# Optimization experiments

Hardware: AMD Instinct MI355X
Metric: run time of the kernel (lower is better)

## Reference

```python
import jax, jax.numpy as jnp
import numpy as np

N_NODES = 50000
N_EDGES = 800000
IN_DIM = 2
EDGE_DIM = 2
HIDDEN = 64
N_LAYERS = 3
MAX_LEAKS = 3


def setup_inputs() -> dict:
    key = jax.random.key(0)
    ks = iter(jax.random.split(key, 32))
    s = 0.05
    inp = {
        "x": jax.random.normal(next(ks), (N_NODES, IN_DIM), dtype=jnp.float32),
        "edge_index": jax.random.randint(next(ks), (2, N_EDGES), 0, N_NODES, dtype=jnp.int32),
        "edge_attr": jax.random.normal(next(ks), (N_EDGES, EDGE_DIM), dtype=jnp.float32),
        # input projection
        "W_in": jax.random.normal(next(ks), (IN_DIM, HIDDEN), dtype=jnp.float32) * s,
        "b_in": jnp.zeros((HIDDEN,), jnp.float32),
        # message-passing layers (stacked over L)
        "W_msg": jax.random.normal(next(ks), (N_LAYERS, HIDDEN + EDGE_DIM, HIDDEN), dtype=jnp.float32) * s,
        "b_msg": jnp.zeros((N_LAYERS, HIDDEN), jnp.float32),
        "W_upd": jax.random.normal(next(ks), (N_LAYERS, 2 * HIDDEN, HIDDEN), dtype=jnp.float32) * s,
        "b_upd": jnp.zeros((N_LAYERS, HIDDEN), jnp.float32),
        # per-node leak-logit head
        "W_node": jax.random.normal(next(ks), (HIDDEN, 1), dtype=jnp.float32) * s,
        "b_node": jnp.zeros((1,), jnp.float32),
        # global no-leak head
        "W_pool": jax.random.normal(next(ks), (HIDDEN, 1), dtype=jnp.float32) * s,
        "b_pool": jnp.zeros((1,), jnp.float32),
        # num_leaks head: Linear(H, H//2) -> ReLU -> Linear(H//2, max_leaks+1)
        "W_h1": jax.random.normal(next(ks), (HIDDEN, HIDDEN // 2), dtype=jnp.float32) * s,
        "b_h1": jnp.zeros((HIDDEN // 2,), jnp.float32),
        "W_h2": jax.random.normal(next(ks), (HIDDEN // 2, MAX_LEAKS + 1), dtype=jnp.float32) * s,
        "b_h2": jnp.zeros((MAX_LEAKS + 1,), jnp.float32),
    }
    return inp


def _run_gnn(x, src, dst, edge_attr, W_in, b_in, W_msg, b_msg, W_upd, b_upd):
    """input_proj + num_layers of message passing; returns node embeddings h [N, H]."""
    n_nodes = x.shape[0]
    h = x @ W_in + b_in  # [N, H]
    # in-degree for mean aggregation (clamped to avoid div-by-zero)
    deg = jax.ops.segment_sum(jnp.ones((src.shape[0],), h.dtype), dst, num_segments=n_nodes)
    deg = jnp.maximum(deg, 1.0)[:, None]  # [N, 1]
    for l in range(N_LAYERS):
        # message: MLP over [h_src || edge_attr], gathered along edges
        m = jax.nn.relu(jnp.concatenate([h[src], edge_attr], axis=-1) @ W_msg[l] + b_msg[l])  # [E, H]
        agg = jax.ops.segment_sum(m, dst, num_segments=n_nodes) / deg  # [N, H]
        # update: MLP over [h || agg]
        h = jax.nn.relu(jnp.concatenate([h, agg], axis=-1) @ W_upd[l] + b_upd[l])  # [N, H]
    return h


def reference(x, edge_index, edge_attr, W_in, b_in, W_msg, b_msg, W_upd, b_upd,
              W_node, b_node, W_pool, b_pool, W_h1, b_h1, W_h2, b_h2):
    src, dst = edge_index[0], edge_index[1]
    # base GNN forward (dropout is identity at inference)
    h = _run_gnn(x, src, dst, edge_attr, W_in, b_in, W_msg, b_msg, W_upd, b_upd)  # [N, H]
    node_logits = (h @ W_node + b_node)[:, 0]          # [N]
    node_probs = jax.nn.sigmoid(node_logits)           # [N]
    # the multi-leak forward re-runs input_proj + mp_layers; identical math -> reuse h
    h_global = jnp.mean(h, axis=0, keepdims=True)      # [1, H]
    num_leaks_logits = jax.nn.relu(h_global @ W_h1 + b_h1) @ W_h2 + b_h2  # [1, max_leaks+1]
    return node_probs, num_leaks_logits, h
```

## Files before the change

kernel.cpp:

```cpp
#include <hip/hip_runtime.h>
#include <math.h>

constexpr int H = 64;

typedef __attribute__((ext_vector_type(8))) short bf16x8;
typedef __attribute__((ext_vector_type(4))) float f32x4;
typedef unsigned long long u64;

__device__ inline unsigned short f2bf(float f) {
  union { float f; unsigned int u; } c; c.f = f;
  unsigned int u = c.u;
  return (unsigned short)((u + 0x7FFF + ((u >> 16) & 1)) >> 16);
}
__device__ inline float bf2f(unsigned int s) {
  union { unsigned int u; float f; } c; c.u = s << 16;
  return c.f;
}
__device__ inline unsigned char f2fp8(float f) {
  return (unsigned char)(__builtin_amdgcn_cvt_pk_fp8_f32(f, f, 0, false) & 0xFF);
}

__global__ void k_prep(int* __restrict__ hist, float* __restrict__ hsumP,
                       const float* __restrict__ Wmsg, const float* __restrict__ Wupd,
                       unsigned short* __restrict__ WmT, unsigned short* __restrict__ WuT,
                       int n) {
  int t = blockIdx.x * blockDim.x + threadIdx.x;
  if (t < n) hist[t] = 0;
  if (t < 512) hsumP[t] = 0.f;
  int u = t - n;
  if (u >= 0 && u < 3 * 12288) {
    int l = u / 12288, rem = u % 12288;
    if (rem < 4096) {
      int j = rem >> 6, k = rem & 63;
      WmT[l * 4096 + rem] = f2bf(Wmsg[(size_t)l * 66 * 64 + k * 64 + j]);
    } else {
      int r2 = rem - 4096;
      int j = r2 >> 7, k = r2 & 127;
      WuT[l * 8192 + r2] = f2bf(Wupd[(size_t)l * 128 * 64 + k * 64 + j]);
    }
  }
}

__global__ void k_hist(const int* __restrict__ dst, int* __restrict__ hist, int E) {
  int e = blockIdx.x * blockDim.x + threadIdx.x;
  if (e < E) atomicAdd(&hist[dst[e]], 1);
}

__global__ void k_scan1(const int* __restrict__ hist, int* __restrict__ bsum, int n) {
  __shared__ int sred[256];
  int tid = threadIdx.x;
  int base = blockIdx.x * 1024 + tid * 4;
  int s = 0;
#pragma unroll
  for (int k = 0; k < 4; ++k) { int i = base + k; if (i < n) s += hist[i]; }
  sred[tid] = s;
  __syncthreads();
  for (int d = 128; d > 0; d >>= 1) {
    if (tid < d) sred[tid] += sred[tid + d];
    __syncthreads();
  }
  if (tid == 0) bsum[blockIdx.x] = sred[0];
}

__global__ void k_scan2(int* __restrict__ bsum, int* __restrict__ bcur, int nb) {
  __shared__ int sd[1024];
  int tid = threadIdx.x;
  int v = (tid < nb) ? bsum[tid] : 0;
  sd[tid] = v;
  __syncthreads();
  for (int d = 1; d < 1024; d <<= 1) {
    int t = (tid >= d) ? sd[tid - d] : 0;
    __syncthreads();
    sd[tid] += t;
    __syncthreads();
  }
  if (tid < nb) {
    int ex = sd[tid] - v;
    bsum[tid] = ex;
    bcur[tid] = ex;
  }
}

__global__ void k_scan3(const int* __restrict__ hist, const int* __restrict__ bsum,
                        int* __restrict__ row_ptr, int* __restrict__ pos, int n) {
  __shared__ int sth[256];
  int tid = threadIdx.x;
  int base = blockIdx.x * 1024 + tid * 4;
  int v[4]; int s = 0;
#pragma unroll
  for (int k = 0; k < 4; ++k) { int i = base + k; v[k] = (i < n) ? hist[i] : 0; s += v[k]; }
  sth[tid] = s;
  __syncthreads();
  for (int d = 1; d < 256; d <<= 1) {
    int t = (tid >= d) ? sth[tid - d] : 0;
    __syncthreads();
    sth[tid] += t;
    __syncthreads();
  }
  int run = bsum[blockIdx.x] + sth[tid] - s;
  if (blockIdx.x == 0 && tid == 0) row_ptr[0] = 0;
#pragma unroll
  for (int k = 0; k < 4; ++k) {
    int i = base + k;
    if (i < n) {
      pos[i] = run;
      run += v[k];
      row_ptr[i + 1] = run;
    }
  }
}

__global__ void k_part(const int* __restrict__ src, const int* __restrict__ dst,
                       const float2* __restrict__ ea2, int* __restrict__ bcur,
                       u64* __restrict__ staged, int E, int B) {
  __shared__ u64 srt[2048];
  __shared__ int cnt[64], offs[64], gbase[64];
  int tid = threadIdx.x;
  int base = blockIdx.x * 2048;
  if (tid < 64) cnt[tid] = 0;
  __syncthreads();
  u64 rec_[8]; int bk_[8], rk_[8];
#pragma unroll
  for (int k = 0; k < 8; ++k) {
    int e = base + k * 256 + tid;
    if (e < E) {
      int d = dst[e];
      int bk = d >> 10;
      float2 eav = ea2[e];
      unsigned int eap = (unsigned int)f2bf(eav.x) | ((unsigned int)f2bf(eav.y) << 16);
      rec_[k] = (u64)(unsigned int)(src[e] & 0xFFFF)
              | ((u64)(unsigned int)(d & 1023) << 16)
              | ((u64)(unsigned int)bk << 26)
              | ((u64)eap << 32);
      bk_[k] = bk;
      rk_[k] = atomicAdd(&cnt[bk], 1);
    } else bk_[k] = -1;
  }
  __syncthreads();
  if (tid == 0) {
    int run = 0;
    for (int b = 0; b < B; ++b) { offs[b] = run; run += cnt[b]; }
  }
  __syncthreads();
#pragma unroll
  for (int k = 0; k < 8; ++k)
    if (bk_[k] >= 0) srt[offs[bk_[k]] + rk_[k]] = rec_[k];
  __syncthreads();
  if (tid < B && cnt[tid] > 0) gbase[tid] = atomicAdd(&bcur[tid], cnt[tid]);
  __syncthreads();
  int total = (base + 2048 <= E) ? 2048 : (E > base ? E - base : 0);
  for (int i = tid; i < total; i += 256) {
    u64 r = srt[i];
    int bk = (int)((r >> 26) & 63u);
    staged[gbase[bk] + (i - offs[bk])] = r;
  }
}

__global__ void k_place(const u64* __restrict__ staged, const int* __restrict__ rptr,
                        u64* __restrict__ erec, int N_) {
  __shared__ int cnt2[1024];
  __shared__ int rptrL[1025];
  int b = blockIdx.x;
  int nd0 = b << 10;
  int nn = min(nd0 + 1024, N_) - nd0;
  int tid = threadIdx.x;
  if (tid < nn) { cnt2[tid] = 0; rptrL[tid] = rptr[nd0 + tid]; }
  if (tid == 0) rptrL[nn] = rptr[nd0 + nn];
  __syncthreads();
  int beg = rptrL[0], end = rptrL[nn];
  for (int i = beg + tid; i < end; i += 1024) {
    u64 r = staged[i];
    int dl = (int)((r >> 16) & 1023u);
    int p = rptrL[dl] + atomicAdd(&cnt2[dl], 1);
    erec[p] = (r & 0xFFFFull) | ((r >> 32) << 32);
  }
}

__global__ void k_scatter(const int* __restrict__ src, const int* __restrict__ dst,
                          const float* __restrict__ ea, int* __restrict__ pos,
                          u64* __restrict__ erec, int E) {
  int e = blockIdx.x * blockDim.x + threadIdx.x;
  if (e < E) {
    int d = dst[e];
    int p = atomicAdd(&pos[d], 1);
    u64 lo = f2bf(ea[2 * e]);
    u64 hi = f2bf(ea[2 * e + 1]);
    erec[p] = (u64)(unsigned int)src[e] | ((lo | (hi << 16)) << 32);
  }
}

__global__ void k_inproj_gemm(const float* __restrict__ x, const float* __restrict__ Win,
                              const float* __restrict__ bin,
                              const unsigned short* __restrict__ wmt,
                              unsigned short* __restrict__ hb,
                              unsigned char* __restrict__ g, int n) {
  int lane = threadIdx.x & 63;
  int wv = blockIdx.x * (blockDim.x >> 6) + (threadIdx.x >> 6);
  int v0 = wv * 16;
  if (v0 >= n) return;
  int r16 = lane & 15, hi = lane >> 4;
  int row = v0 + r16;
  float x0 = 0.f, x1 = 0.f;
  if (row < n) { x0 = x[2 * row]; x1 = x[2 * row + 1]; }
  union { bf16x8 v; unsigned short u[8]; } af[2];
#pragma unroll
  for (int s = 0; s < 2; ++s)
#pragma unroll
    for (int t = 0; t < 8; ++t) {
      int j = s * 32 + hi * 8 + t;
      af[s].u[t] = f2bf(fmaf(x0, Win[j], fmaf(x1, Win[64 + j], bin[j])));
    }
  if (row < n) {
    *(bf16x8*)(hb + (size_t)row * H + hi * 8)      = af[0].v;
    *(bf16x8*)(hb + (size_t)row * H + 32 + hi * 8) = af[1].v;
  }
  bf16x8 bfr[2][4];
#pragma unroll
  for (int ks = 0; ks < 2; ++ks)
#pragma unroll
    for (int jt = 0; jt < 4; ++jt)
      bfr[ks][jt] = *(const bf16x8*)(wmt + (jt * 16 + r16) * 64 + ks * 32 + hi * 8);
  f32x4 acc[4] = {};
#pragma unroll
  for (int ks = 0; ks < 2; ++ks)
#pragma unroll
    for (int jt = 0; jt < 4; ++jt)
      acc[jt] = __builtin_amdgcn_mfma_f32_16x16x32_bf16(af[ks].v, bfr[ks][jt], acc[jt], 0, 0, 0);
#pragma unroll
  for (int jt = 0; jt < 4; ++jt) {
    int col = jt * 16 + r16;
#pragma unroll
    for (int r = 0; r < 4; ++r) {
      int orow = v0 + hi * 4 + r;
      if (orow < n) g[(size_t)orow * H + col] = f2fp8(acc[jt][r]);
    }
  }
}

__device__ inline void acc8(float* a, uint2 gw, float e0, float e1,
                            const float4 waL, const float4 waH,
                            const float4 wbL, const float4 wbH,
                            const float4 bL, const float4 bH) {
  a[0] += fmaxf(fmaf(e0, waL.x, fmaf(e1, wbL.x, __builtin_amdgcn_cvt_f32_fp8(gw.x, 0) + bL.x)), 0.f);
  a[1] += fmaxf(fmaf(e0, waL.y, fmaf(e1, wbL.y, __builtin_amdgcn_cvt_f32_fp8(gw.x, 1) + bL.y)), 0.f);
  a[2] += fmaxf(fmaf(e0, waL.z, fmaf(e1, wbL.z, __builtin_amdgcn_cvt_f32_fp8(gw.x, 2) + bL.z)), 0.f);
  a[3] += fmaxf(fmaf(e0, waL.w, fmaf(e1, wbL.w, __builtin_amdgcn_cvt_f32_fp8(gw.x, 3) + bL.w)), 0.f);
  a[4] += fmaxf(fmaf(e0, waH.x, fmaf(e1, wbH.x, __builtin_amdgcn_cvt_f32_fp8(gw.y, 0) + bH.x)), 0.f);
  a[5] += fmaxf(fmaf(e0, waH.y, fmaf(e1, wbH.y, __builtin_amdgcn_cvt_f32_fp8(gw.y, 1) + bH.y)), 0.f);
  a[6] += fmaxf(fmaf(e0, waH.z, fmaf(e1, wbH.z, __builtin_amdgcn_cvt_f32_fp8(gw.y, 2) + bH.z)), 0.f);
  a[7] += fmaxf(fmaf(e0, waH.w, fmaf(e1, wbH.w, __builtin_amdgcn_cvt_f32_fp8(gw.y, 3) + bH.w)), 0.f);
}

__global__ void k_layer(const unsigned char* __restrict__ g_in,
                        const int* __restrict__ row_ptr, const u64* __restrict__ erec,
                        const float* __restrict__ Wm2, const float* __restrict__ bm,
                        unsigned short* __restrict__ hb,
                        const unsigned short* __restrict__ wut,
                        const float* __restrict__ bu,
                        const unsigned short* __restrict__ wmt_next,
                        unsigned char* __restrict__ g_out,
                        float* __restrict__ hout,
                        const float* __restrict__ Wn, const float* __restrict__ bn,
                        float* __restrict__ probs, float* __restrict__ hsumP,
                        int n) {
  __shared__ __align__(16) unsigned short aggL[64][72];
  __shared__ __align__(16) unsigned short hstage[4][16][72];
  __shared__ float shsum[64];
  int v0 = blockIdx.x * 64;

  {
    int gid = threadIdx.x >> 3, r = threadIdx.x & 7;
    int j0 = r * 8;
    float4 waL = *(const float4*)(Wm2 + j0);
    float4 waH = *(const float4*)(Wm2 + j0 + 4);
    float4 wbL = *(const float4*)(Wm2 + 64 + j0);
    float4 wbH = *(const float4*)(Wm2 + 64 + j0 + 4);
    float4 bL  = *(const float4*)(bm + j0);
    float4 bH  = *(const float4*)(bm + j0 + 4);
#pragma unroll
    for (int it = 0; it < 2; ++it) {
      int lv = it * 32 + gid;
      int v = v0 + lv;
      uint4 o = make_uint4(0, 0, 0, 0);
      if (v < n) {
        int beg = row_ptr[v], end = row_ptr[v + 1];
        float a[8] = {0.f, 0.f, 0.f, 0.f, 0.f, 0.f, 0.f, 0.f};
        int i = beg;
        for (; i + 3 < end; i += 4) {
          u64 rA = erec[i], rB = erec[i + 1], rC = erec[i + 2], rD = erec[i + 3];
          uint2 gwA = *(const uint2*)(g_in + (size_t)(unsigned int)rA * H + j0);
          uint2 gwB = *(const uint2*)(g_in + (size_t)(unsigned int)rB * H + j0);
          uint2 gwC = *(const uint2*)(g_in + (size_t)(unsigned int)rC * H + j0);
          uint2 gwD = *(const uint2*)(g_in + (size_t)(unsigned int)rD * H + j0);
          unsigned int eA = (unsigned int)(rA >> 32), eB = (unsigned int)(rB >> 32);
          unsigned int eC = (unsigned int)(rC >> 32), eD = (unsigned int)(rD >> 32);
          acc8(a, gwA, bf2f(eA & 0xffffu), bf2f(eA >> 16), waL, waH, wbL, wbH, bL, bH);
          acc8(a, gwB, bf2f(eB & 0xffffu), bf2f(eB >> 16), waL, waH, wbL, wbH, bL, bH);
          acc8(a, gwC, bf2f(eC & 0xffffu), bf2f(eC >> 16), waL, waH, wbL, wbH, bL, bH);
          acc8(a, gwD, bf2f(eD & 0xffffu), bf2f(eD >> 16), waL, waH, wbL, wbH, bL, bH);
        }
        for (; i < end; ++i) {
          u64 rA = erec[i];
          uint2 gwA = *(const uint2*)(g_in + (size_t)(unsigned int)rA * H + j0);
          unsigned int eA = (unsigned int)(rA >> 32);
          acc8(a, gwA, bf2f(eA & 0xffffu), bf2f(eA >> 16), waL, waH, wbL, wbH, bL, bH);
        }
        float inv = 1.f / fmaxf((float)(end - beg), 1.f);
        o.x = (unsigned int)f2bf(a[0] * inv) | ((unsigned int)f2bf(a[1] * inv) << 16);
        o.y = (unsigned int)f2bf(a[2] * inv) | ((unsigned int)f2bf(a[3] * inv) << 16);
        o.z = (unsigned int)f2bf(a[4] * inv) | ((unsigned int)f2bf(a[5] * inv) << 16);
        o.w = (unsigned int)f2bf(a[6] * inv) | ((unsigned int)f2bf(a[7] * inv) << 16);
      }
      *(uint4*)(&aggL[lv][j0]) = o;
    }
  }
  __syncthreads();

  int lane = threadIdx.x & 63;
  int w = threadIdx.x >> 6;
  int wv0 = v0 + w * 16;
  bool act = wv0 < n;
  int r16 = lane & 15, hi = lane >> 4;
  int lw = w * 16 + r16;
  if (hout && threadIdx.x < 64) shsum[threadIdx.x] = 0.f;
  bf16x8 bfr[4][4];
#pragma unroll
  for (int ks = 0; ks < 4; ++ks)
#pragma unroll
    for (int jt = 0; jt < 4; ++jt)
      bfr[ks][jt] = *(const bf16x8*)(wut + (jt * 16 + r16) * 128 + ks * 32 + hi * 8);
  f32x4 acc[4];
#pragma unroll
  for (int jt = 0; jt < 4; ++jt) {
    float b = bu[jt * 16 + r16];
    acc[jt] = (f32x4){b, b, b, b};
  }
  bf16x8 afr[4];
  int row = wv0 + r16;
  if (act && row < n) {
    const unsigned short* hrow = hb + (size_t)row * H + hi * 8;
    afr[0] = *(const bf16x8*)(hrow);
    afr[1] = *(const bf16x8*)(hrow + 32);
  } else {
    afr[0] = afr[1] = (bf16x8){0,0,0,0,0,0,0,0};
  }
  afr[2] = *(const bf16x8*)(&aggL[lw][hi * 8]);
  afr[3] = *(const bf16x8*)(&aggL[lw][32 + hi * 8]);
#pragma unroll
  for (int ks = 0; ks < 4; ++ks)
#pragma unroll
    for (int jt = 0; jt < 4; ++jt)
      acc[jt] = __builtin_amdgcn_mfma_f32_16x16x32_bf16(afr[ks], bfr[ks][jt], acc[jt], 0, 0, 0);
  float ov[4][4];
  unsigned short ob[4][4];
#pragma unroll
  for (int jt = 0; jt < 4; ++jt) {
    int col = jt * 16 + r16;
#pragma unroll
    for (int r = 0; r < 4; ++r) {
      int orow = wv0 + hi * 4 + r;
      bool ok = act && orow < n;
      float o = fmaxf(acc[jt][r], 0.f);
      ov[jt][r] = ok ? o : 0.f;
      ob[jt][r] = f2bf(ov[jt][r]);
      if (ok) {
        hb[(size_t)orow * H + col] = ob[jt][r];
        if (hout) hout[(size_t)orow * H + col] = o;
      }
    }
  }
  if (wmt_next) {
#pragma unroll
    for (int jt = 0; jt < 4; ++jt)
#pragma unroll
      for (int r = 0; r < 4; ++r)
        hstage[w][hi * 4 + r][jt * 16 + r16] = ob[jt][r];
    __syncthreads();
    bf16x8 af2[2];
    af2[0] = *(const bf16x8*)(&hstage[w][r16][hi * 8]);
    af2[1] = *(const bf16x8*)(&hstage[w][r16][32 + hi * 8]);
    bf16x8 bf2r[2][4];
#pragma unroll
    for (int ks = 0; ks < 2; ++ks)
#pragma unroll
      for (int jt = 0; jt < 4; ++jt)
        bf2r[ks][jt] = *(const bf16x8*)(wmt_next + (jt * 16 + r16) * 64 + ks * 32 + hi * 8);
    f32x4 acc2[4] = {};
#pragma unroll
    for (int ks = 0; ks < 2; ++ks)
#pragma unroll
      for (int jt = 0; jt < 4; ++jt)
        acc2[jt] = __builtin_amdgcn_mfma_f32_16x16x32_bf16(af2[ks], bf2r[ks][jt], acc2[jt], 0, 0, 0);
#pragma unroll
    for (int jt = 0; jt < 4; ++jt) {
      int col = jt * 16 + r16;
#pragma unroll
      for (int r = 0; r < 4; ++r) {
        int orow = wv0 + hi * 4 + r;
        if (act && orow < n) g_out[(size_t)orow * H + col] = f2fp8(acc2[jt][r]);
      }
    }
  } else {
    float bn0 = bn[0];
    float lg[4] = {0.f, 0.f, 0.f, 0.f};
#pragma unroll
    for (int jt = 0; jt < 4; ++jt) {
      float wn = Wn[jt * 16 + r16];
#pragma unroll
      for (int r = 0; r < 4; ++r) lg[r] = fmaf(ov[jt][r], wn, lg[r]);
    }
#pragma unroll
    for (int d = 1; d < 16; d <<= 1) {
#pragma unroll
      for (int r = 0; r < 4; ++r) lg[r] += __shfl_xor(lg[r], d);
    }
    if (r16 == 0) {
#pragma unroll
      for (int r = 0; r < 4; ++r) {
        int orow = wv0 + hi * 4 + r;
        if (act && orow < n) probs[orow] = 1.f / (1.f + expf(-(lg[r] + bn0)));
      }
    }
    __syncthreads();
#pragma unroll
    for (int jt = 0; jt < 4; ++jt) {
      float s = ov[jt][0] + ov[jt][1] + ov[jt][2] + ov[jt][3];
      s += __shfl_xor(s, 16); s += __shfl_xor(s, 32);
      if (hi == 0) atomicAdd(&shsum[jt * 16 + r16], s);
    }
    __syncthreads();
    if (threadIdx.x < 64)
      atomicAdd(&hsumP[((blockIdx.x & 7) << 6) + threadIdx.x], shsum[threadIdx.x]);
  }
}

__global__ void k_final(const float* __restrict__ hsumP,
                        const float* __restrict__ W1, const float* __restrict__ b1,
                        const float* __restrict__ W2, const float* __restrict__ b2,
                        float* __restrict__ out4, float n_nodes) {
  __shared__ float hmean[64];
  __shared__ float z1[32];
  int tid = threadIdx.x;
  if (tid < 64) {
    float s = 0.f;
#pragma unroll
    for (int b = 0; b < 8; ++b) s += hsumP[b * 64 + tid];
    hmean[tid] = s / n_nodes;
  }
  __syncthreads();
  if (tid < 32) {
    float a = b1[tid];
    for (int k = 0; k < 64; ++k) a = fmaf(hmean[k], W1[k * 32 + tid], a);
    z1[tid] = fmaxf(a, 0.f);
  }
  __syncthreads();
  if (tid < 4) {
    float a = b2[tid];
    for (int k = 0; k < 32; ++k) a = fmaf(z1[k], W2[k * 4 + tid], a);
    out4[tid] = a;
  }
}

extern "C" void kernel_launch(void* const* d_in, const int* in_sizes, int n_in,
                              void* d_out, int out_size, void* d_ws, size_t ws_size,
                              hipStream_t stream) {
  const float* x    = (const float*)d_in[0];
  const int*   ei   = (const int*)d_in[1];
  const float* ea   = (const float*)d_in[2];
  const float* Win  = (const float*)d_in[3];
  const float* bin  = (const float*)d_in[4];
  const float* Wmsg = (const float*)d_in[5];
  const float* bmsg = (const float*)d_in[6];
  const float* Wupd = (const float*)d_in[7];
  const float* bupd = (const float*)d_in[8];
  const float* Wn   = (const float*)d_in[9];
  const float* bn   = (const float*)d_in[10];
  const float* W1   = (const float*)d_in[13];
  const float* b1   = (const float*)d_in[14];
  const float* W2   = (const float*)d_in[15];
  const float* b2   = (const float*)d_in[16];

  const int N = in_sizes[0] / 2;
  const int E = in_sizes[1] / 2;
  const int* src = ei;
  const int* dst = ei + E;

  char* ws = (char*)d_ws;
  size_t off = 0;
  auto alloc = [&](size_t bytes) {
    void* p = ws + off;
    off = (off + bytes + 255) & ~(size_t)255;
    return p;
  };
  int*   hist = (int*)  alloc((size_t)N * 4);
  int*   rptr = (int*)  alloc((size_t)(N + 1) * 4);
  int*   pos  = (int*)  alloc((size_t)N * 4);
  int*   bsum = (int*)  alloc((size_t)1024 * 4);
  int*   bcur = (int*)  alloc((size_t)1024 * 4);
  u64*   staged = (u64*)alloc((size_t)E * 8);
  u64*   erec = (u64*)  alloc((size_t)E * 8);
  unsigned short* hb   = (unsigned short*)alloc((size_t)N * H * 2);
  unsigned char*  gA   = (unsigned char*) alloc((size_t)N * H);
  unsigned char*  gB   = (unsigned char*) alloc((size_t)N * H);
  unsigned short* WmT  = (unsigned short*)alloc((size_t)3 * 64 * 64 * 2);
  unsigned short* WuT  = (unsigned short*)alloc((size_t)3 * 64 * 128 * 2);
  float* hsumP = (float*)alloc(8 * 64 * 4);
  (void)ws_size;

  float* probs = (float*)d_out;
  float* out4  = probs + N;
  float* h     = out4 + 4;

  int eb = (E + 255) / 256;
  int sb = (N + 1023) / 1024;
  k_prep<<<(N + 3 * 12288 + 255) / 256, 256, 0, stream>>>(hist, hsumP, Wmsg, Wupd, WmT, WuT, N);
  k_hist<<<eb, 256, 0, stream>>>(dst, hist, E);
  k_scan1<<<sb, 256, 0, stream>>>(hist, bsum, N);
  k_scan2<<<1, 1024, 0, stream>>>(bsum, bcur, sb);
  k_scan3<<<sb, 256, 0, stream>>>(hist, bsum, rptr, pos, N);

  int B = (N + 1023) >> 10;
  if (B <= 64) {
    k_part<<<(E + 2047) / 2048, 256, 0, stream>>>(src, dst, (const float2*)ea,
                                                  bcur, staged, E, B);
    k_place<<<B, 1024, 0, stream>>>(staged, rptr, erec, N);
  } else {
    k_scatter<<<eb, 256, 0, stream>>>(src, dst, ea, pos, erec, E);
  }

  int tiles = (N + 15) / 16;
  int mb = (tiles + 3) / 4;
  k_inproj_gemm<<<mb, 256, 0, stream>>>(x, Win, bin, WmT, hb, gA, N);

  int lb = (N + 63) / 64;
  for (int l = 0; l < 3; ++l) {
    const unsigned char* gin = (l & 1) ? gB : gA;
    unsigned char* gout      = (l & 1) ? gA : gB;
    k_layer<<<lb, 256, 0, stream>>>(gin, rptr, erec,
                                    Wmsg + (size_t)l * 66 * 64 + 64 * 64,
                                    bmsg + (size_t)l * 64,
                                    hb, WuT + (size_t)l * 64 * 128,
                                    bupd + (size_t)l * 64,
                                    (l < 2) ? (WmT + (size_t)(l + 1) * 64 * 64) : nullptr,
                                    gout,
                                    (l == 2) ? h : nullptr,
                                    Wn, bn, probs, hsumP, N);
  }

  k_final<<<1, 64, 0, stream>>>(hsumP, W1, b1, W2, b2, out4, (float)N);
}
```

Before: 215.9 us.

## Fuse degree histogram into bucket partition and halve nodes per layer block

```diff
diff --git a/kernel.cpp b/kernel.cpp
--- a/kernel.cpp
+++ b/kernel.cpp
@@ -21,12 +21,14 @@
 }
 
 __global__ void k_prep(int* __restrict__ hist, float* __restrict__ hsumP,
+                       int* __restrict__ bcur2,
                        const float* __restrict__ Wmsg, const float* __restrict__ Wupd,
                        unsigned short* __restrict__ WmT, unsigned short* __restrict__ WuT,
                        int n) {
   int t = blockIdx.x * blockDim.x + threadIdx.x;
   if (t < n) hist[t] = 0;
   if (t < 512) hsumP[t] = 0.f;
+  if (t < 64) bcur2[t] = 0;
   int u = t - n;
   if (u >= 0 && u < 3 * 12288) {
     int l = u / 12288, rem = u % 12288;
@@ -62,7 +64,7 @@
   if (tid == 0) bsum[blockIdx.x] = sred[0];
 }
 
-__global__ void k_scan2(int* __restrict__ bsum, int* __restrict__ bcur, int nb) {
+__global__ void k_scan2(int* __restrict__ bsum, int nb) {
   __shared__ int sd[1024];
   int tid = threadIdx.x;
   int v = (tid < nb) ? bsum[tid] : 0;
@@ -74,11 +76,7 @@
     sd[tid] += t;
     __syncthreads();
   }
-  if (tid < nb) {
-    int ex = sd[tid] - v;
-    bsum[tid] = ex;
-    bcur[tid] = ex;
-  }
+  if (tid < nb) bsum[tid] = sd[tid] - v;
 }
 
 __global__ void k_scan3(const int* __restrict__ hist, const int* __restrict__ bsum,
@@ -111,8 +109,9 @@
 }
 
 __global__ void k_part(const int* __restrict__ src, const int* __restrict__ dst,
-                       const float2* __restrict__ ea2, int* __restrict__ bcur,
-                       u64* __restrict__ staged, int E, int B) {
+                       const float2* __restrict__ ea2,
+                       int* __restrict__ hist, int* __restrict__ bcur2,
+                       u64* __restrict__ staged, int E, int B, int C) {
   __shared__ u64 srt[2048];
   __shared__ int cnt[64], offs[64], gbase[64];
   int tid = threadIdx.x;
@@ -125,6 +124,7 @@
     int e = base + k * 256 + tid;
     if (e < E) {
       int d = dst[e];
+      atomicAdd(&hist[d], 1);
       int bk = d >> 10;
       float2 eav = ea2[e];
       unsigned int eap = (unsigned int)f2bf(eav.x) | ((unsigned int)f2bf(eav.y) << 16);
@@ -146,18 +146,19 @@
   for (int k = 0; k < 8; ++k)
     if (bk_[k] >= 0) srt[offs[bk_[k]] + rk_[k]] = rec_[k];
   __syncthreads();
-  if (tid < B && cnt[tid] > 0) gbase[tid] = atomicAdd(&bcur[tid], cnt[tid]);
+  if (tid < B && cnt[tid] > 0) gbase[tid] = atomicAdd(&bcur2[tid], cnt[tid]);
   __syncthreads();
   int total = (base + 2048 <= E) ? 2048 : (E > base ? E - base : 0);
   for (int i = tid; i < total; i += 256) {
     u64 r = srt[i];
     int bk = (int)((r >> 26) & 63u);
-    staged[gbase[bk] + (i - offs[bk])] = r;
-  }
-}
-
-__global__ void k_place(const u64* __restrict__ staged, const int* __restrict__ rptr,
-                        u64* __restrict__ erec, int N_) {
+    staged[(size_t)bk * C + gbase[bk] + (i - offs[bk])] = r;
+  }
+}
+
+__global__ void k_place(const u64* __restrict__ staged, const int* __restrict__ bcur2,
+                        const int* __restrict__ rptr,
+                        u64* __restrict__ erec, int N_, int C) {
   __shared__ int cnt2[1024];
   __shared__ int rptrL[1025];
   int b = blockIdx.x;
@@ -167,9 +168,10 @@
   if (tid < nn) { cnt2[tid] = 0; rptrL[tid] = rptr[nd0 + tid]; }
   if (tid == 0) rptrL[nn] = rptr[nd0 + nn];
   __syncthreads();
-  int beg = rptrL[0], end = rptrL[nn];
-  for (int i = beg + tid; i < end; i += 1024) {
-    u64 r = staged[i];
+  int count = bcur2[b];
+  const u64* sb = staged + (size_t)b * C;
+  for (int i = tid; i < count; i += 1024) {
+    u64 r = sb[i];
     int dl = (int)((r >> 16) & 1023u);
     int p = rptrL[dl] + atomicAdd(&cnt2[dl], 1);
     erec[p] = (r & 0xFFFFull) | ((r >> 32) << 32);
@@ -263,10 +265,10 @@
                         const float* __restrict__ Wn, const float* __restrict__ bn,
                         float* __restrict__ probs, float* __restrict__ hsumP,
                         int n) {
-  __shared__ __align__(16) unsigned short aggL[64][72];
-  __shared__ __align__(16) unsigned short hstage[4][16][72];
+  __shared__ __align__(16) unsigned short aggL[32][72];
+  __shared__ __align__(16) unsigned short hstage[2][16][72];
   __shared__ float shsum[64];
-  int v0 = blockIdx.x * 64;
+  int v0 = blockIdx.x * 32;
 
   {
     int gid = threadIdx.x >> 3, r = threadIdx.x & 7;
@@ -277,51 +279,47 @@
     float4 wbH = *(const float4*)(Wm2 + 64 + j0 + 4);
     float4 bL  = *(const float4*)(bm + j0);
     float4 bH  = *(const float4*)(bm + j0 + 4);
-#pragma unroll
-    for (int it = 0; it < 2; ++it) {
-      int lv = it * 32 + gid;
-      int v = v0 + lv;
-      uint4 o = make_uint4(0, 0, 0, 0);
-      if (v < n) {
-        int beg = row_ptr[v], end = row_ptr[v + 1];
-        float a[8] = {0.f, 0.f, 0.f, 0.f, 0.f, 0.f, 0.f, 0.f};
-        int i = beg;
-        for (; i + 3 < end; i += 4) {
-          u64 rA = erec[i], rB = erec[i + 1], rC = erec[i + 2], rD = erec[i + 3];
-          uint2 gwA = *(const uint2*)(g_in + (size_t)(unsigned int)rA * H + j0);
-          uint2 gwB = *(const uint2*)(g_in + (size_t)(unsigned int)rB * H + j0);
-          uint2 gwC = *(const uint2*)(g_in + (size_t)(unsigned int)rC * H + j0);
-          uint2 gwD = *(const uint2*)(g_in + (size_t)(unsigned int)rD * H + j0);
-          unsigned int eA = (unsigned int)(rA >> 32), eB = (unsigned int)(rB >> 32);
-          unsigned int eC = (unsigned int)(rC >> 32), eD = (unsigned int)(rD >> 32);
-          acc8(a, gwA, bf2f(eA & 0xffffu), bf2f(eA >> 16), waL, waH, wbL, wbH, bL, bH);
-          acc8(a, gwB, bf2f(eB & 0xffffu), bf2f(eB >> 16), waL, waH, wbL, wbH, bL, bH);
-          acc8(a, gwC, bf2f(eC & 0xffffu), bf2f(eC >> 16), waL, waH, wbL, wbH, bL, bH);
-          acc8(a, gwD, bf2f(eD & 0xffffu), bf2f(eD >> 16), waL, waH, wbL, wbH, bL, bH);
-        }
-        for (; i < end; ++i) {
-          u64 rA = erec[i];
-          uint2 gwA = *(const uint2*)(g_in + (size_t)(unsigned int)rA * H + j0);
-          unsigned int eA = (unsigned int)(rA >> 32);
-          acc8(a, gwA, bf2f(eA & 0xffffu), bf2f(eA >> 16), waL, waH, wbL, wbH, bL, bH);
-        }
-        float inv = 1.f / fmaxf((float)(end - beg), 1.f);
-        o.x = (unsigned int)f2bf(a[0] * inv) | ((unsigned int)f2bf(a[1] * inv) << 16);
-        o.y = (unsigned int)f2bf(a[2] * inv) | ((unsigned int)f2bf(a[3] * inv) << 16);
-        o.z = (unsigned int)f2bf(a[4] * inv) | ((unsigned int)f2bf(a[5] * inv) << 16);
-        o.w = (unsigned int)f2bf(a[6] * inv) | ((unsigned int)f2bf(a[7] * inv) << 16);
+    int v = v0 + gid;
+    uint4 o = make_uint4(0, 0, 0, 0);
+    if (v < n) {
+      int beg = row_ptr[v], end = row_ptr[v + 1];
+      float a[8] = {0.f, 0.f, 0.f, 0.f, 0.f, 0.f, 0.f, 0.f};
+      int i = beg;
+      for (; i + 3 < end; i += 4) {
+        u64 rA = erec[i], rB = erec[i + 1], rC = erec[i + 2], rD = erec[i + 3];
+        uint2 gwA = *(const uint2*)(g_in + (size_t)(unsigned int)rA * H + j0);
+        uint2 gwB = *(const uint2*)(g_in + (size_t)(unsigned int)rB * H + j0);
+        uint2 gwC = *(const uint2*)(g_in + (size_t)(unsigned int)rC * H + j0);
+        uint2 gwD = *(const uint2*)(g_in + (size_t)(unsigned int)rD * H + j0);
+        unsigned int eA = (unsigned int)(rA >> 32), eB = (unsigned int)(rB >> 32);
+        unsigned int eC = (unsigned int)(rC >> 32), eD = (unsigned int)(rD >> 32);
+        acc8(a, gwA, bf2f(eA & 0xffffu), bf2f(eA >> 16), waL, waH, wbL, wbH, bL, bH);
+        acc8(a, gwB, bf2f(eB & 0xffffu), bf2f(eB >> 16), waL, waH, wbL, wbH, bL, bH);
+        acc8(a, gwC, bf2f(eC & 0xffffu), bf2f(eC >> 16), waL, waH, wbL, wbH, bL, bH);
+        acc8(a, gwD, bf2f(eD & 0xffffu), bf2f(eD >> 16), waL, waH, wbL, wbH, bL, bH);
       }
-      *(uint4*)(&aggL[lv][j0]) = o;
-    }
+      for (; i < end; ++i) {
+        u64 rA = erec[i];
+        uint2 gwA = *(const uint2*)(g_in + (size_t)(unsigned int)rA * H + j0);
+        unsigned int eA = (unsigned int)(rA >> 32);
+        acc8(a, gwA, bf2f(eA & 0xffffu), bf2f(eA >> 16), waL, waH, wbL, wbH, bL, bH);
+      }
+      float inv = 1.f / fmaxf((float)(end - beg), 1.f);
+      o.x = (unsigned int)f2bf(a[0] * inv) | ((unsigned int)f2bf(a[1] * inv) << 16);
+      o.y = (unsigned int)f2bf(a[2] * inv) | ((unsigned int)f2bf(a[3] * inv) << 16);
+      o.z = (unsigned int)f2bf(a[4] * inv) | ((unsigned int)f2bf(a[5] * inv) << 16);
+      o.w = (unsigned int)f2bf(a[6] * inv) | ((unsigned int)f2bf(a[7] * inv) << 16);
+    }
+    *(uint4*)(&aggL[gid][j0]) = o;
   }
   __syncthreads();
 
   int lane = threadIdx.x & 63;
   int w = threadIdx.x >> 6;
+  bool mw = (w < 2);
   int wv0 = v0 + w * 16;
-  bool act = wv0 < n;
+  bool act = mw && (wv0 < n);
   int r16 = lane & 15, hi = lane >> 4;
-  int lw = w * 16 + r16;
   if (hout && threadIdx.x < 64) shsum[threadIdx.x] = 0.f;
   bf16x8 bfr[4][4];
 #pragma unroll
@@ -344,8 +342,13 @@
   } else {
     afr[0] = afr[1] = (bf16x8){0,0,0,0,0,0,0,0};
   }
-  afr[2] = *(const bf16x8*)(&aggL[lw][hi * 8]);
-  afr[3] = *(const bf16x8*)(&aggL[lw][32 + hi * 8]);
+  if (mw) {
+    int lw = w * 16 + r16;
+    afr[2] = *(const bf16x8*)(&aggL[lw][hi * 8]);
+    afr[3] = *(const bf16x8*)(&aggL[lw][32 + hi * 8]);
+  } else {
+    afr[2] = afr[3] = (bf16x8){0,0,0,0,0,0,0,0};
+  }
 #pragma unroll
   for (int ks = 0; ks < 4; ++ks)
 #pragma unroll
@@ -370,34 +373,38 @@
     }
   }
   if (wmt_next) {
-#pragma unroll
-    for (int jt = 0; jt < 4; ++jt)
-#pragma unroll
-      for (int r = 0; r < 4; ++r)
-        hstage[w][hi * 4 + r][jt * 16 + r16] = ob[jt][r];
-    __syncthreads();
-    bf16x8 af2[2];
-    af2[0] = *(const bf16x8*)(&hstage[w][r16][hi * 8]);
-    af2[1] = *(const bf16x8*)(&hstage[w][r16][32 + hi * 8]);
-    bf16x8 bf2r[2][4];
-#pragma unroll
-    for (int ks = 0; ks < 2; ++ks)
+    if (mw) {
 #pragma unroll
       for (int jt = 0; jt < 4; ++jt)
-        bf2r[ks][jt] = *(const bf16x8*)(wmt_next + (jt * 16 + r16) * 64 + ks * 32 + hi * 8);
-    f32x4 acc2[4] = {};
-#pragma unroll
-    for (int ks = 0; ks < 2; ++ks)
-#pragma unroll
-      for (int jt = 0; jt < 4; ++jt)
-        acc2[jt] = __builtin_amdgcn_mfma_f32_16x16x32_bf16(af2[ks], bf2r[ks][jt], acc2[jt], 0, 0, 0);
-#pragma unroll
-    for (int jt = 0; jt < 4; ++jt) {
-      int col = jt * 16 + r16;
-#pragma unroll
-      for (int r = 0; r < 4; ++r) {
-        int orow = wv0 + hi * 4 + r;
-        if (act && orow < n) g_out[(size_t)orow * H + col] = f2fp8(acc2[jt][r]);
+#pragma unroll
+        for (int r = 0; r < 4; ++r)
+          hstage[w][hi * 4 + r][jt * 16 + r16] = ob[jt][r];
+    }
+    __syncthreads();
+    if (mw) {
+      bf16x8 af2[2];
+      af2[0] = *(const bf16x8*)(&hstage[w][r16][hi * 8]);
+      af2[1] = *(const bf16x8*)(&hstage[w][r16][32 + hi * 8]);
+      bf16x8 bf2r[2][4];
+#pragma unroll
+      for (int ks = 0; ks < 2; ++ks)
+#pragma unroll
+        for (int jt = 0; jt < 4; ++jt)
+          bf2r[ks][jt] = *(const bf16x8*)(wmt_next + (jt * 16 + r16) * 64 + ks * 32 + hi * 8);
+      f32x4 acc2[4] = {};
+#pragma unroll
+      for (int ks = 0; ks < 2; ++ks)
+#pragma unroll
+        for (int jt = 0; jt < 4; ++jt)
+          acc2[jt] = __builtin_amdgcn_mfma_f32_16x16x32_bf16(af2[ks], bf2r[ks][jt], acc2[jt], 0, 0, 0);
+#pragma unroll
+      for (int jt = 0; jt < 4; ++jt) {
+        int col = jt * 16 + r16;
+#pragma unroll
+        for (int r = 0; r < 4; ++r) {
+          int orow = wv0 + hi * 4 + r;
+          if (act && orow < n) g_out[(size_t)orow * H + col] = f2fp8(acc2[jt][r]);
+        }
       }
     }
   } else {
@@ -414,11 +421,11 @@
 #pragma unroll
       for (int r = 0; r < 4; ++r) lg[r] += __shfl_xor(lg[r], d);
     }
-    if (r16 == 0) {
+    if (r16 == 0 && act) {
 #pragma unroll
       for (int r = 0; r < 4; ++r) {
         int orow = wv0 + hi * 4 + r;
-        if (act && orow < n) probs[orow] = 1.f / (1.f + expf(-(lg[r] + bn0)));
+        if (orow < n) probs[orow] = 1.f / (1.f + expf(-(lg[r] + bn0)));
       }
     }
     __syncthreads();
@@ -485,6 +492,9 @@
   const int* src = ei;
   const int* dst = ei + E;
 
+  const int B = (N + 1023) >> 10;
+  const int C = (2 * (E / (B > 0 ? B : 1)) + 2048 + 255) & ~255;
+
   char* ws = (char*)d_ws;
   size_t off = 0;
   auto alloc = [&](size_t bytes) {
@@ -492,13 +502,13 @@
     off = (off + bytes + 255) & ~(size_t)255;
     return p;
   };
-  int*   hist = (int*)  alloc((size_t)N * 4);
-  int*   rptr = (int*)  alloc((size_t)(N + 1) * 4);
-  int*   pos  = (int*)  alloc((size_t)N * 4);
-  int*   bsum = (int*)  alloc((size_t)1024 * 4);
-  int*   bcur = (int*)  alloc((size_t)1024 * 4);
-  u64*   staged = (u64*)alloc((size_t)E * 8);
-  u64*   erec = (u64*)  alloc((size_t)E * 8);
+  int*   hist  = (int*)  alloc((size_t)N * 4);
+  int*   rptr  = (int*)  alloc((size_t)(N + 1) * 4);
+  int*   pos   = (int*)  alloc((size_t)N * 4);
+  int*   bsum  = (int*)  alloc((size_t)1024 * 4);
+  int*   bcur2 = (int*)  alloc((size_t)64 * 4);
+  u64*   staged = (u64*) alloc((size_t)(B <= 64 ? 64 : 0) * C * 8 + 8);
+  u64*   erec  = (u64*)  alloc((size_t)E * 8);
   unsigned short* hb   = (unsigned short*)alloc((size_t)N * H * 2);
   unsigned char*  gA   = (unsigned char*) alloc((size_t)N * H);
   unsigned char*  gB   = (unsigned char*) alloc((size_t)N * H);
@@ -513,18 +523,20 @@
 
   int eb = (E + 255) / 256;
   int sb = (N + 1023) / 1024;
-  k_prep<<<(N + 3 * 12288 + 255) / 256, 256, 0, stream>>>(hist, hsumP, Wmsg, Wupd, WmT, WuT, N);
-  k_hist<<<eb, 256, 0, stream>>>(dst, hist, E);
-  k_scan1<<<sb, 256, 0, stream>>>(hist, bsum, N);
-  k_scan2<<<1, 1024, 0, stream>>>(bsum, bcur, sb);
-  k_scan3<<<sb, 256, 0, stream>>>(hist, bsum, rptr, pos, N);
-
-  int B = (N + 1023) >> 10;
+  k_prep<<<(N + 3 * 12288 + 255) / 256, 256, 0, stream>>>(hist, hsumP, bcur2,
+                                                          Wmsg, Wupd, WmT, WuT, N);
   if (B <= 64) {
     k_part<<<(E + 2047) / 2048, 256, 0, stream>>>(src, dst, (const float2*)ea,
-                                                  bcur, staged, E, B);
-    k_place<<<B, 1024, 0, stream>>>(staged, rptr, erec, N);
+                                                  hist, bcur2, staged, E, B, C);
+    k_scan1<<<sb, 256, 0, stream>>>(hist, bsum, N);
+    k_scan2<<<1, 1024, 0, stream>>>(bsum, sb);
+    k_scan3<<<sb, 256, 0, stream>>>(hist, bsum, rptr, pos, N);
+    k_place<<<B, 1024, 0, stream>>>(staged, bcur2, rptr, erec, N, C);
   } else {
+    k_hist<<<eb, 256, 0, stream>>>(dst, hist, E);
+    k_scan1<<<sb, 256, 0, stream>>>(hist, bsum, N);
+    k_scan2<<<1, 1024, 0, stream>>>(bsum, sb);
+    k_scan3<<<sb, 256, 0, stream>>>(hist, bsum, rptr, pos, N);
     k_scatter<<<eb, 256, 0, stream>>>(src, dst, ea, pos, erec, E);
   }
 
@@ -532,7 +544,7 @@
   int mb = (tiles + 3) / 4;
   k_inproj_gemm<<<mb, 256, 0, stream>>>(x, Win, bin, WmT, hb, gA, N);
 
-  int lb = (N + 63) / 64;
+  int lb = (N + 31) / 32;
   for (int l = 0; l < 3; ++l) {
     const unsigned char* gin = (l & 1) ? gB : gA;
     unsigned char* gout      = (l & 1) ? gA : gB;
```

Measured after the change: 214.9 us, median of 2. About the same (-0.4%).
